# Performance work log

Measured on AMD Instinct MI355X. Metric: run time of the kernel, lower is better.

The kernel has to match this reference:

```python
import jax, jax.numpy as jnp
import numpy as np

K = 4096          # infeatures
N = 12288         # outfeatures
M = 4096          # tokens (batch*seq)
GROUPSIZE = 128
G = K // GROUPSIZE  # 32 groups
PACK = 8          # 8 int4 nibbles per int32


def _unpack_int4(q):
    """Unpack int32 [R, C] -> int32 [R, C*8]; nibble j of word c maps to column c*8+j."""
    shifts = jnp.arange(0, 32, 4, dtype=jnp.int32)          # [8]
    nib = (q[:, :, None] >> shifts[None, None, :]) & 0xF    # [R, C, 8]
    return nib.reshape(q.shape[0], -1)


def setup_inputs() -> dict:
    key = jax.random.key(0)
    k1, k2, k3, k4, k5 = jax.random.split(key, 5)
    x = jax.random.normal(k1, (M, K), dtype=jnp.float32)
    qweight = jax.random.randint(k2, (K, N // PACK), 0, 2147483647, dtype=jnp.int32)
    qzeros = jax.random.randint(k3, (G, N // PACK), 0, 2147483647, dtype=jnp.int32)
    scales = jax.random.uniform(k4, (G, N), dtype=jnp.float32, minval=0.001, maxval=0.01)
    bias = jax.random.normal(k5, (N,), dtype=jnp.float32)
    return {"x": x, "qweight": qweight, "qzeros": qzeros, "scales": scales,
            "bias": bias, "groupsize": GROUPSIZE}


def reference(x, qweight, qzeros, scales, bias, groupsize):
    # Dequantize: w[k, n] = (q4[k, n] - z4[k//gs, n]) * scales[k//gs, n]
    w_int = _unpack_int4(qweight)                 # [K, N] int32, values 0..15
    z_int = _unpack_int4(qzeros)                  # [G, N] int32 (+1 already folded in)
    z_full = jnp.repeat(z_int, groupsize, axis=0)      # [K, N]
    s_full = jnp.repeat(scales, groupsize, axis=0)     # [K, N]
    weight = (w_int - z_full).astype(x.dtype) * s_full  # [K, N]
    out = x @ weight + bias                        # [M, N]
    return out
```

## Files before the change

kernel.cpp:

```cpp
#include <hip/hip_runtime.h>

#define M_DIM 4096
#define N_DIM 12288
#define K_DIM 4096
#define NP    1536
#define GS    128

typedef unsigned short ushort_t;
typedef _Float16 half8 __attribute__((ext_vector_type(8)));
typedef unsigned short us8 __attribute__((ext_vector_type(8)));
typedef float f32x16 __attribute__((ext_vector_type(16)));
typedef float f32x4 __attribute__((ext_vector_type(4)));

__device__ __forceinline__ unsigned short f2h(float f) {
  _Float16 h = (_Float16)f;
  return __builtin_bit_cast(unsigned short, h);
}

#define GLDS16(G, L) __builtin_amdgcn_global_load_lds(                      \
    (const __attribute__((address_space(1))) void*)(G),                     \
    (__attribute__((address_space(3))) void*)(L), 16, 0, 0)

#define DQ_BLOCKS (96 * 64)
#define CVT_BLOCKS (M_DIM * K_DIM / 8 / 256)

__global__ __launch_bounds__(256) void prep_kernel(
    const int* __restrict__ qw, const int* __restrict__ qz,
    const float* __restrict__ sc, ushort_t* __restrict__ wt,
    const float* __restrict__ x, ushort_t* __restrict__ xb) {
  __shared__ int ldsQ[64 * 16];
  __shared__ int ldsZ[16];
  const int tid = threadIdx.x;
  if (blockIdx.x >= DQ_BLOCKS) {
    int cid = (blockIdx.x - DQ_BLOCKS) * 256 + tid;
    const float4* p = (const float4*)(x + (size_t)cid * 8);
    float4 a = p[0], b = p[1];
    us8 o;
    o[0] = f2h(a.x); o[1] = f2h(a.y); o[2] = f2h(a.z); o[3] = f2h(a.w);
    o[4] = f2h(b.x); o[5] = f2h(b.y); o[6] = f2h(b.z); o[7] = f2h(b.w);
    *(us8*)(xb + (size_t)cid * 8) = o;
    return;
  }
  const int bx = blockIdx.x % 96;
  const int by = blockIdx.x / 96;
  const int k0 = by * 64;
  const int n0 = bx * 128;
  const int w0 = n0 >> 3;
  const int g  = k0 >> 7;
#pragma unroll
  for (int i = 0; i < 4; ++i) {
    int idx = i * 256 + tid;
    int row = idx >> 4, w = idx & 15;
    ldsQ[row * 16 + (w ^ (row & 15))] = qw[(size_t)(k0 + row) * NP + w0 + w];
  }
  if (tid < 16) ldsZ[tid] = qz[g * NP + w0 + tid];
  __syncthreads();
  const int nl  = tid >> 1;
  const int kh  = tid & 1;
  const int col = nl >> 3;
  const int j4  = (nl & 7) * 4;
  const int z   = (ldsZ[col] >> j4) & 0xF;
  const float s = sc[(size_t)g * N_DIM + n0 + nl];
  ushort_t* dst = wt + (size_t)(n0 + nl) * K_DIM + k0 + kh * 32;
#pragma unroll
  for (int c = 0; c < 4; ++c) {
    us8 o;
#pragma unroll
    for (int ii = 0; ii < 8; ++ii) {
      int row = kh * 32 + c * 8 + ii;
      int q = (ldsQ[row * 16 + (col ^ (row & 15))] >> j4) & 0xF;
      o[ii] = f2h((float)(q - z) * s);
    }
    *(us8*)(dst + c * 8) = o;
  }
}


__device__ __forceinline__ void stage_unit(
    int u, const ushort_t* __restrict__ Ag, const ushort_t* __restrict__ Bg,
    int m0, int n0, int tid, ushort_t* lds) {
  const int t   = u >> 1;
  const int ks  = u & 1;
  const int b   = t & 1;
  const int kbu = t * 64 + ks * 32;
  const int r   = tid >> 1;
  const int hp  = (tid & 1) ^ ((tid >> 3) & 1);
  const size_t ka = (size_t)kbu + hp * 8;
  ushort_t* dA = lds + b * 32768 + (2 * ks) * 4096 + tid * 8;
  ushort_t* dB = dA + 16384;
  const ushort_t* sA = Ag + (size_t)(m0 + r) * K_DIM + ka;
  const ushort_t* sB = Bg + (size_t)(n0 + r) * K_DIM + ka;
  GLDS16(sA,      dA);
  GLDS16(sA + 16, dA + 4096);
  GLDS16(sB,      dB);
  GLDS16(sB + 16, dB + 4096);
}

template <int VN, bool STG>
__device__ __forceinline__ void gemm_phase(
    int p, const ushort_t* __restrict__ Ag, const ushort_t* __restrict__ Bg,
    int m0, int n0, int tid, ushort_t* lds, f32x4 (&acc)[8][4]) {
  const int lane = tid & 63;
  const int wid  = tid >> 6;
  const int wm   = wid & 1;
  const int wn   = wid >> 1;
  const int ks   = p & 1;
  const int b    = (p >> 1) & 1;
  const int c  = lane >> 4;
  const int rl = lane & 15;
  const int sg = (c & 1) ^ ((rl >> 2) & 1);
  const ushort_t* base = lds + b * 32768 + (2 * ks + (c >> 1)) * 4096 + sg * 8;
  const ushort_t* pa = base + (wm * 128 + rl) * 16;
  const ushort_t* pb = base + 16384 + (wn * 64 + rl) * 16;
  half8 af[8], bf[4];
#pragma unroll
  for (int i = 0; i < 8; ++i) af[i] = *(const half8*)(pa + i * 256);
#pragma unroll
  for (int j = 0; j < 4; ++j) bf[j] = *(const half8*)(pb + j * 256);
  if constexpr (STG) stage_unit(p + 3, Ag, Bg, m0, n0, tid, lds);
  __builtin_amdgcn_s_barrier();
  asm volatile("s_waitcnt lgkmcnt(0)" ::: "memory");
  __builtin_amdgcn_sched_barrier(0);
  __builtin_amdgcn_s_setprio(1);
#pragma unroll
  for (int i = 0; i < 8; ++i)
#pragma unroll
    for (int j = 0; j < 4; ++j)
      acc[i][j] = __builtin_amdgcn_mfma_f32_16x16x32_f16(af[i], bf[j],
                                                         acc[i][j], 0, 0, 0);
  __builtin_amdgcn_s_setprio(0);
  if constexpr (VN == 8)      asm volatile("s_waitcnt vmcnt(8)" ::: "memory");
  else if constexpr (VN == 4) asm volatile("s_waitcnt vmcnt(4)" ::: "memory");
  else if constexpr (VN == 0) asm volatile("s_waitcnt vmcnt(0)" ::: "memory");
  if constexpr (VN >= 0) {
    __builtin_amdgcn_s_barrier();
    asm volatile("" ::: "memory");
  }
}

__global__ __launch_bounds__(512, 2) void gemm256_kernel(
    const ushort_t* __restrict__ Xb, const ushort_t* __restrict__ Wt,
    const float* __restrict__ bias, float* __restrict__ out) {
  __shared__ __align__(16) ushort_t lds[65536];
  const int tid = threadIdx.x;
  const int m0  = blockIdx.x * 256;
  const int n0  = blockIdx.y * 256;
  f32x4 acc[8][4] = {};

  stage_unit(0, Xb, Wt, m0, n0, tid, lds);
  stage_unit(1, Xb, Wt, m0, n0, tid, lds);
  stage_unit(2, Xb, Wt, m0, n0, tid, lds);
  asm volatile("s_waitcnt vmcnt(8)" ::: "memory");
  __builtin_amdgcn_s_barrier();
  asm volatile("" ::: "memory");

#pragma unroll 4
  for (int p = 0; p < 124; ++p)
    gemm_phase<8, true>(p, Xb, Wt, m0, n0, tid, lds, acc);
  gemm_phase<8, true >(124, Xb, Wt, m0, n0, tid, lds, acc);
  gemm_phase<4, false>(125, Xb, Wt, m0, n0, tid, lds, acc);
  gemm_phase<0, false>(126, Xb, Wt, m0, n0, tid, lds, acc);
  gemm_phase<-1, false>(127, Xb, Wt, m0, n0, tid, lds, acc);

  const int lane = tid & 63;
  const int wm   = (tid >> 6) & 1;
  const int wn   = tid >> 7;
#pragma unroll
  for (int jj = 0; jj < 4; ++jj) {
    int n = n0 + wn * 64 + jj * 16 + (lane & 15);
    float bv = bias[n];
#pragma unroll
    for (int i = 0; i < 8; ++i) {
      int mb = (int)(m0 + wm * 128 + i * 16 + ((lane >> 4) << 2));
#pragma unroll
      for (int r = 0; r < 4; ++r)
        __builtin_nontemporal_store(acc[i][jj][r] + bv,
                                    out + (size_t)(mb + r) * N_DIM + n);
    }
  }
}

template <int APRE, int BPRE>
__global__ __launch_bounds__(256) void gemm_kernel(
    const ushort_t* __restrict__ Xb, const float* __restrict__ Xf,
    const ushort_t* __restrict__ Wt,
    const int* __restrict__ qw, const int* __restrict__ qz,
    const float* __restrict__ sc,
    const float* __restrict__ bias, float* __restrict__ out) {
  __shared__ __align__(16) ushort_t lsA[128 * 64];
  __shared__ __align__(16) ushort_t lsB[128 * 64];
  const int tid  = threadIdx.x;
  const int lane = tid & 63;
  const int wid  = tid >> 6;
  const int wm   = wid & 1;
  const int wn   = wid >> 1;
  const int m0   = blockIdx.x * 128;
  const int n0   = blockIdx.y * 128;

  f32x16 acc[2][2] = {};

  for (int kt = 0; kt < K_DIM / 64; ++kt) {
    const int kb = kt * 64;
    if constexpr (APRE) {
#pragma unroll
      for (int i = 0; i < 4; ++i) {
        int cid = i * 256 + tid;
        int r = cid >> 3, scol = cid & 7;
        int c = scol ^ (r & 7);
        GLDS16(Xb + (size_t)(m0 + r) * K_DIM + kb + c * 8, lsA + cid * 8);
      }
    } else {
#pragma unroll
      for (int i = 0; i < 4; ++i) {
        int cid = i * 256 + tid;
        int r = cid >> 3, scol = cid & 7;
        int c = scol ^ (r & 7);
        const float* src = Xf + (size_t)(m0 + r) * K_DIM + kb + c * 8;
        float4 a = *(const float4*)src;
        float4 b = *(const float4*)(src + 4);
        us8 o;
        o[0] = f2h(a.x); o[1] = f2h(a.y); o[2] = f2h(a.z); o[3] = f2h(a.w);
        o[4] = f2h(b.x); o[5] = f2h(b.y); o[6] = f2h(b.z); o[7] = f2h(b.w);
        *(us8*)(lsA + cid * 8) = o;
      }
    }
    if constexpr (BPRE) {
#pragma unroll
      for (int i = 0; i < 4; ++i) {
        int cid = i * 256 + tid;
        int r = cid >> 3, scol = cid & 7;
        int c = scol ^ (r & 7);
        GLDS16(Wt + (size_t)(n0 + r) * K_DIM + kb + c * 8, lsB + cid * 8);
      }
    } else {
#pragma unroll
      for (int i = 0; i < 4; ++i) {
        int wi = i * 256 + tid;
        int kl = wi >> 4, cw = wi & 15;
        int k = kb + kl;
        int g = k >> 7;
        int qword = qw[(size_t)k * NP + (n0 >> 3) + cw];
        int zword = qz[g * NP + (n0 >> 3) + cw];
        float4 s0 = *(const float4*)(sc + (size_t)g * N_DIM + n0 + cw * 8);
        float4 s1 = *(const float4*)(sc + (size_t)g * N_DIM + n0 + cw * 8 + 4);
        float sv[8] = {s0.x, s0.y, s0.z, s0.w, s1.x, s1.y, s1.z, s1.w};
#pragma unroll
        for (int j = 0; j < 8; ++j) {
          int nl = cw * 8 + j;
          int q = (qword >> (4 * j)) & 0xF;
          int z = (zword >> (4 * j)) & 0xF;
          lsB[nl * 64 + (((kl >> 3) ^ (nl & 7)) << 3) + (kl & 7)] =
              f2h((float)(q - z) * sv[j]);
        }
      }
    }
    __syncthreads();
#pragma unroll
    for (int ks = 0; ks < 4; ++ks) {
      half8 af[2], bfr[2];
      const int h = lane >> 5;
      const int c = ks * 2 + h;
#pragma unroll
      for (int i = 0; i < 2; ++i) {
        int row = wm * 64 + i * 32 + (lane & 31);
        af[i] = *(const half8*)(lsA + (row * 8 + (c ^ (row & 7))) * 8);
      }
#pragma unroll
      for (int jj = 0; jj < 2; ++jj) {
        int row = wn * 64 + jj * 32 + (lane & 31);
        bfr[jj] = *(const half8*)(lsB + (row * 8 + (c ^ (row & 7))) * 8);
      }
#pragma unroll
      for (int i = 0; i < 2; ++i)
#pragma unroll
        for (int jj = 0; jj < 2; ++jj)
          acc[i][jj] = __builtin_amdgcn_mfma_f32_32x32x16_f16(
              af[i], bfr[jj], acc[i][jj], 0, 0, 0);
    }
    __syncthreads();
  }

#pragma unroll
  for (int jj = 0; jj < 2; ++jj) {
    int n = n0 + wn * 64 + jj * 32 + (lane & 31);
    float bv = bias[n];
#pragma unroll
    for (int i = 0; i < 2; ++i) {
      int mbase = m0 + wm * 64 + i * 32 + ((lane >> 5) << 2);
#pragma unroll
      for (int reg = 0; reg < 16; ++reg) {
        int m = mbase + (reg & 3) + ((reg >> 2) << 3);
        __builtin_nontemporal_store(acc[i][jj][reg] + bv,
                                    out + (size_t)m * N_DIM + n);
      }
    }
  }
}

extern "C" void kernel_launch(void* const* d_in, const int* in_sizes, int n_in,
                              void* d_out, int out_size, void* d_ws, size_t ws_size,
                              hipStream_t stream) {
  const float* x    = (const float*)d_in[0];
  const int*   qw   = (const int*)d_in[1];
  const int*   qz   = (const int*)d_in[2];
  const float* sc   = (const float*)d_in[3];
  const float* bias = (const float*)d_in[4];
  float*       out  = (float*)d_out;

  const size_t WT_BYTES = (size_t)N_DIM * K_DIM * 2;
  const size_t XB_BYTES = (size_t)M_DIM * K_DIM * 2;
  ushort_t* Wt = (ushort_t*)d_ws;
  ushort_t* Xb = (ushort_t*)((char*)d_ws + WT_BYTES);
  const bool hasWt = ws_size >= WT_BYTES;
  const bool hasXb = ws_size >= WT_BYTES + XB_BYTES;

  if (hasXb) {
    prep_kernel<<<DQ_BLOCKS + CVT_BLOCKS, 256, 0, stream>>>(qw, qz, sc, Wt, x, Xb);
    dim3 grid256(M_DIM / 256, N_DIM / 256);
    gemm256_kernel<<<grid256, 512, 0, stream>>>(Xb, Wt, bias, out);
  } else if (hasWt) {
    dim3 grid(M_DIM / 128, N_DIM / 128);
    prep_kernel<<<DQ_BLOCKS, 256, 0, stream>>>(qw, qz, sc, Wt, x, nullptr);
    gemm_kernel<0, 1><<<grid, 256, 0, stream>>>(nullptr, x, Wt, qw, qz, sc, bias, out);
  } else {
    dim3 grid(M_DIM / 128, N_DIM / 128);
    gemm_kernel<0, 0><<<grid, 256, 0, stream>>>(nullptr, x, nullptr, qw, qz, sc, bias, out);
  }
}
```

Baseline: 668.7 us.

## Interleave LDS fragment loads with MFMAs via staged lgkmcnt waits

The GEMM phase now issues LDS fragment reads in a fixed order and waits on lgkmcnt incrementally before each MFMA row, so matrix math starts before all fragments have arrived. The barrier that previously sat between the loads and the MFMAs is removed. The prep kernel also widens the x-to-fp16 conversion to 16 elements per thread and loads packed weights as int4 vectors. Dropping the pre-MFMA barrier relies on the trailing barrier for correctness, and the fixed schedule limits the compiler's freedom to reorder.

```diff
diff --git a/kernel.cpp b/kernel.cpp
--- a/kernel.cpp
+++ b/kernel.cpp
@@ -22,7 +22,7 @@
     (__attribute__((address_space(3))) void*)(L), 16, 0, 0)
 
 #define DQ_BLOCKS (96 * 64)
-#define CVT_BLOCKS (M_DIM * K_DIM / 8 / 256)
+#define CVT_BLOCKS (M_DIM * K_DIM / 16 / 256)
 
 __global__ __launch_bounds__(256) void prep_kernel(
     const int* __restrict__ qw, const int* __restrict__ qz,
@@ -32,13 +32,16 @@
   __shared__ int ldsZ[16];
   const int tid = threadIdx.x;
   if (blockIdx.x >= DQ_BLOCKS) {
-    int cid = (blockIdx.x - DQ_BLOCKS) * 256 + tid;
-    const float4* p = (const float4*)(x + (size_t)cid * 8);
-    float4 a = p[0], b = p[1];
-    us8 o;
-    o[0] = f2h(a.x); o[1] = f2h(a.y); o[2] = f2h(a.z); o[3] = f2h(a.w);
-    o[4] = f2h(b.x); o[5] = f2h(b.y); o[6] = f2h(b.z); o[7] = f2h(b.w);
-    *(us8*)(xb + (size_t)cid * 8) = o;
+    size_t cid = (size_t)(blockIdx.x - DQ_BLOCKS) * 256 + tid;
+    const float4* p = (const float4*)(x + cid * 16);
+    float4 a = p[0], b = p[1], c = p[2], d = p[3];
+    us8 o0, o1;
+    o0[0] = f2h(a.x); o0[1] = f2h(a.y); o0[2] = f2h(a.z); o0[3] = f2h(a.w);
+    o0[4] = f2h(b.x); o0[5] = f2h(b.y); o0[6] = f2h(b.z); o0[7] = f2h(b.w);
+    o1[0] = f2h(c.x); o1[1] = f2h(c.y); o1[2] = f2h(c.z); o1[3] = f2h(c.w);
+    o1[4] = f2h(d.x); o1[5] = f2h(d.y); o1[6] = f2h(d.z); o1[7] = f2h(d.w);
+    *(us8*)(xb + cid * 16)     = o0;
+    *(us8*)(xb + cid * 16 + 8) = o1;
     return;
   }
   const int bx = blockIdx.x % 96;
@@ -47,11 +50,13 @@
   const int n0 = bx * 128;
   const int w0 = n0 >> 3;
   const int g  = k0 >> 7;
-#pragma unroll
-  for (int i = 0; i < 4; ++i) {
-    int idx = i * 256 + tid;
-    int row = idx >> 4, w = idx & 15;
-    ldsQ[row * 16 + (w ^ (row & 15))] = qw[(size_t)(k0 + row) * NP + w0 + w];
+  {
+    int row = tid >> 2, qc = tid & 3;
+    int4 v = *(const int4*)(qw + (size_t)(k0 + row) * NP + w0 + qc * 4);
+    ldsQ[row * 16 + ((qc * 4 + 0) ^ (row & 15))] = v.x;
+    ldsQ[row * 16 + ((qc * 4 + 1) ^ (row & 15))] = v.y;
+    ldsQ[row * 16 + ((qc * 4 + 2) ^ (row & 15))] = v.z;
+    ldsQ[row * 16 + ((qc * 4 + 3) ^ (row & 15))] = v.w;
   }
   if (tid < 16) ldsZ[tid] = qz[g * NP + w0 + tid];
   __syncthreads();
@@ -96,6 +101,21 @@
   GLDS16(sB + 16, dB + 4096);
 }
 
+template <int N>
+__device__ __forceinline__ void wait_lgkm() {
+  if constexpr (N == 0)      asm volatile("s_waitcnt lgkmcnt(0)" ::: "memory");
+  else if constexpr (N == 1) asm volatile("s_waitcnt lgkmcnt(1)" ::: "memory");
+  else if constexpr (N == 2) asm volatile("s_waitcnt lgkmcnt(2)" ::: "memory");
+  else if constexpr (N == 3) asm volatile("s_waitcnt lgkmcnt(3)" ::: "memory");
+  else if constexpr (N == 4) asm volatile("s_waitcnt lgkmcnt(4)" ::: "memory");
+  else if constexpr (N == 5) asm volatile("s_waitcnt lgkmcnt(5)" ::: "memory");
+  else if constexpr (N == 6) asm volatile("s_waitcnt lgkmcnt(6)" ::: "memory");
+  else if constexpr (N == 7) asm volatile("s_waitcnt lgkmcnt(7)" ::: "memory");
+  __builtin_amdgcn_sched_barrier(0);
+}
+
+#define SB() __builtin_amdgcn_sched_barrier(0)
+
 template <int VN, bool STG>
 __device__ __forceinline__ void gemm_phase(
     int p, const ushort_t* __restrict__ Ag, const ushort_t* __restrict__ Bg,
@@ -113,21 +133,36 @@
   const ushort_t* pa = base + (wm * 128 + rl) * 16;
   const ushort_t* pb = base + 16384 + (wn * 64 + rl) * 16;
   half8 af[8], bf[4];
-#pragma unroll
-  for (int i = 0; i < 8; ++i) af[i] = *(const half8*)(pa + i * 256);
-#pragma unroll
-  for (int j = 0; j < 4; ++j) bf[j] = *(const half8*)(pb + j * 256);
+  af[0] = *(const half8*)(pa);
+  bf[0] = *(const half8*)(pb);
+  bf[1] = *(const half8*)(pb + 256);
+  bf[2] = *(const half8*)(pb + 512);
+  bf[3] = *(const half8*)(pb + 768);
+  SB();
+  af[1] = *(const half8*)(pa + 256);  SB();
+  af[2] = *(const half8*)(pa + 512);  SB();
+  af[3] = *(const half8*)(pa + 768);  SB();
+  af[4] = *(const half8*)(pa + 1024); SB();
+  af[5] = *(const half8*)(pa + 1280); SB();
+  af[6] = *(const half8*)(pa + 1536); SB();
+  af[7] = *(const half8*)(pa + 1792); SB();
   if constexpr (STG) stage_unit(p + 3, Ag, Bg, m0, n0, tid, lds);
-  __builtin_amdgcn_s_barrier();
-  asm volatile("s_waitcnt lgkmcnt(0)" ::: "memory");
-  __builtin_amdgcn_sched_barrier(0);
   __builtin_amdgcn_s_setprio(1);
-#pragma unroll
-  for (int i = 0; i < 8; ++i)
-#pragma unroll
-    for (int j = 0; j < 4; ++j)
-      acc[i][j] = __builtin_amdgcn_mfma_f32_16x16x32_f16(af[i], bf[j],
-                                                         acc[i][j], 0, 0, 0);
+#define MFMA_ROW(i, W)                                                       \
+  wait_lgkm<W>();                                                            \
+  acc[i][0] = __builtin_amdgcn_mfma_f32_16x16x32_f16(af[i], bf[0], acc[i][0], 0, 0, 0); \
+  acc[i][1] = __builtin_amdgcn_mfma_f32_16x16x32_f16(af[i], bf[1], acc[i][1], 0, 0, 0); \
+  acc[i][2] = __builtin_amdgcn_mfma_f32_16x16x32_f16(af[i], bf[2], acc[i][2], 0, 0, 0); \
+  acc[i][3] = __builtin_amdgcn_mfma_f32_16x16x32_f16(af[i], bf[3], acc[i][3], 0, 0, 0)
+  MFMA_ROW(0, 7);
+  MFMA_ROW(1, 6);
+  MFMA_ROW(2, 5);
+  MFMA_ROW(3, 4);
+  MFMA_ROW(4, 3);
+  MFMA_ROW(5, 2);
+  MFMA_ROW(6, 1);
+  MFMA_ROW(7, 0);
+#undef MFMA_ROW
   __builtin_amdgcn_s_setprio(0);
   if constexpr (VN == 8)      asm volatile("s_waitcnt vmcnt(8)" ::: "memory");
   else if constexpr (VN == 4) asm volatile("s_waitcnt vmcnt(4)" ::: "memory");
@@ -155,11 +190,10 @@
   asm volatile("" ::: "memory");
 
 #pragma unroll 4
-  for (int p = 0; p < 124; ++p)
+  for (int p = 0; p < 125; ++p)
     gemm_phase<8, true>(p, Xb, Wt, m0, n0, tid, lds, acc);
-  gemm_phase<8, true >(124, Xb, Wt, m0, n0, tid, lds, acc);
-  gemm_phase<4, false>(125, Xb, Wt, m0, n0, tid, lds, acc);
-  gemm_phase<0, false>(126, Xb, Wt, m0, n0, tid, lds, acc);
+  gemm_phase<4,  false>(125, Xb, Wt, m0, n0, tid, lds, acc);
+  gemm_phase<0,  false>(126, Xb, Wt, m0, n0, tid, lds, acc);
   gemm_phase<-1, false>(127, Xb, Wt, m0, n0, tid, lds, acc);
 
   const int lane = tid & 63;
```

Result: faster. 638.9 us (-4.5%).
